# Kernel optimization log

Measured on AMD Instinct MI355X. Metric: run time of the kernel, lower is better.

Reference implementation:

```python
import jax, jax.numpy as jnp
import numpy as np

B, L, DIM = 2, 2048, 1024
H, D = 16, 64  # n_heads, head_dim; H*D == DIM


def setup_inputs() -> dict:
    key = jax.random.key(0)
    ks = jax.random.split(key, 5)
    s = 0.02
    return {
        "x": jax.random.normal(ks[0], (B, L, DIM), dtype=jnp.float32),
        "Wq": jax.random.normal(ks[1], (DIM, H * D), dtype=jnp.float32) * s,
        "Wk": jax.random.normal(ks[2], (DIM, H * D), dtype=jnp.float32) * s,
        "Wv": jax.random.normal(ks[3], (DIM, H * D), dtype=jnp.float32) * s,
        "Wo": jax.random.normal(ks[4], (H * D, DIM), dtype=jnp.float32) * s,
    }


def reference(x, Wq, Wk, Wv, Wo):
    b, l, _ = x.shape
    scale = 1.0 / np.sqrt(D).astype(np.float32)
    # QKV projections -> [b, h, l, d]
    q = (x @ Wq).reshape(b, l, H, D).transpose(0, 2, 1, 3)
    k = (x @ Wk).reshape(b, l, H, D).transpose(0, 2, 1, 3)
    v = (x @ Wv).reshape(b, l, H, D).transpose(0, 2, 1, 3)
    # dense scores [b, h, l, l]
    scores = jnp.einsum("bhqd,bhkd->bhqk", q, k)
    # diagonal mask: each token cannot attend to itself
    diag = jnp.eye(l, dtype=bool)  # [l, l]
    scores = jnp.where(diag, -jnp.inf, scores)
    attn = jax.nn.softmax(scores * scale, axis=-1)
    out = jnp.einsum("bhqk,bhkd->bhqd", attn, v)
    out = out.transpose(0, 2, 1, 3).reshape(b, l, H * D)
    return out @ Wo
```

## Files before the change

kernel.cpp:

```cpp
#include <hip/hip_runtime.h>
#include <hip/hip_bf16.h>
#include <math.h>

#define L_SEQ 2048
#define DIMN  1024
#define NH    16
#define HD    64
#define NB    2
#define NTOK  (NB * L_SEQ)

typedef __attribute__((ext_vector_type(8))) short bf16x8;
typedef __attribute__((ext_vector_type(4))) float f32x4;
typedef __attribute__((ext_vector_type(4))) short short4v;
typedef __attribute__((ext_vector_type(2))) unsigned uint32x2;

__device__ __forceinline__ short f2bf(float x) {
  return (short)__bfloat16_as_ushort(__float2bfloat16(x));
}

__device__ __forceinline__ unsigned cvt_pk_bf16(float lo, float hi) {
  unsigned r;
  asm("v_cvt_pk_bf16_f32 %0, %1, %2" : "=v"(r) : "v"(lo), "v"(hi));
  return r;
}

__device__ __forceinline__ void gload_lds16(const short* gsrc, char* lds_dst) {
  __builtin_amdgcn_global_load_lds(
      (const __attribute__((address_space(1))) void*)gsrc,
      (__attribute__((address_space(3))) void*)lds_dst, 16, 0, 0);
}

__global__ __launch_bounds__(256) void cast_x_k(const float* __restrict__ in,
                                                short* __restrict__ out) {
  const int i = (blockIdx.x * 256 + threadIdx.x) * 8;
  float4 a = *(const float4*)(in + i);
  float4 b = *(const float4*)(in + i + 4);
  bf16x8 o;
  o[0] = f2bf(a.x); o[1] = f2bf(a.y); o[2] = f2bf(a.z); o[3] = f2bf(a.w);
  o[4] = f2bf(b.x); o[5] = f2bf(b.y); o[6] = f2bf(b.z); o[7] = f2bf(b.w);
  *(bf16x8*)(out + i) = o;
}

__global__ __launch_bounds__(256) void castT_k(const float* __restrict__ W,
                                               short* __restrict__ Wt) {
  __shared__ float s[64][65];
  const int tid = threadIdx.x;
  const int k0 = blockIdx.y * 64, n0 = blockIdx.x * 64;
#pragma unroll
  for (int i = 0; i < 4; ++i) {
    int idx = i * 256 + tid;
    int r = idx >> 4, c = (idx & 15) * 4;
    float4 v = *(const float4*)(W + (size_t)(k0 + r) * DIMN + n0 + c);
    s[r][c] = v.x; s[r][c + 1] = v.y; s[r][c + 2] = v.z; s[r][c + 3] = v.w;
  }
  __syncthreads();
#pragma unroll
  for (int i = 0; i < 4; ++i) {
    int idx = i * 256 + tid;
    int r = idx >> 4, c = (idx & 15) * 4;
    short4v o = { f2bf(s[c][r]), f2bf(s[c + 1][r]), f2bf(s[c + 2][r]), f2bf(s[c + 3][r]) };
    *(short4v*)(Wt + (size_t)(n0 + r) * DIMN + k0 + c) = o;
  }
}

__global__ __launch_bounds__(256) void vT_k(const short* __restrict__ V,
                                            short* __restrict__ Vt) {
  __shared__ short s[64][72];
  const int tid = threadIdx.x;
  const int bh = blockIdx.y;
  const int l0 = blockIdx.x * 64;
  const int row = tid >> 2, c0 = (tid & 3) * 16;
  const short* Vh = V + (size_t)bh * L_SEQ * HD;
  bf16x8 a = *(const bf16x8*)(Vh + (size_t)(l0 + row) * HD + c0);
  bf16x8 b = *(const bf16x8*)(Vh + (size_t)(l0 + row) * HD + c0 + 8);
#pragma unroll
  for (int j = 0; j < 8; ++j) { s[c0 + j][row] = a[j]; s[c0 + 8 + j][row] = b[j]; }
  __syncthreads();
  short* Vth = Vt + (size_t)bh * HD * L_SEQ;
  bf16x8 o0 = *(const bf16x8*)&s[row][c0];
  bf16x8 o1 = *(const bf16x8*)&s[row][c0 + 8];
  *(bf16x8*)(Vth + (size_t)row * L_SEQ + l0 + c0) = o0;
  *(bf16x8*)(Vth + (size_t)row * L_SEQ + l0 + c0 + 8) = o1;
}

template <int MODE>
__global__ __launch_bounds__(256) void mm_k(const short* __restrict__ A,
                                            const short* __restrict__ B0,
                                            const short* __restrict__ B1,
                                            const short* __restrict__ B2,
                                            void* __restrict__ C0,
                                            void* __restrict__ C1,
                                            void* __restrict__ C2,
                                            float scale0) {
  __shared__ char smem[65536];
  const int tid  = threadIdx.x;
  const int lane = tid & 63, wv = tid >> 6;
  const int g = lane >> 4, r16 = lane & 15;
  const int wr = wv >> 1, wc = wv & 1;
  const int row0 = blockIdx.y * 128, col0 = blockIdx.x * 128;
  const int z = blockIdx.z;
  const short* Bt = (z == 0) ? B0 : (z == 1 ? B1 : B2);
  const float scale = (MODE == 0 && z == 0) ? scale0 : 1.0f;

  f32x4 acc[4][4];
#pragma unroll
  for (int mi = 0; mi < 4; ++mi)
#pragma unroll
    for (int ni = 0; ni < 4; ++ni) acc[mi][ni] = (f32x4){0.f, 0.f, 0.f, 0.f};

  auto stage = [&](int buf, int kt) {
    const int k0 = kt * 64;
    char* As = smem + buf * 32768;
    char* Bs = As + 16384;
#pragma unroll
    for (int j = 0; j < 4; ++j) {
      const int o = j * 4096 + wv * 1024 + lane * 16;
      const int row = o >> 7;
      const int slot = (o >> 4) & 7;
      const int ksrc = k0 + ((slot ^ (row & 7)) << 3);
      gload_lds16(A  + (size_t)(row0 + row) * DIMN + ksrc, As + j * 4096 + wv * 1024);
      gload_lds16(Bt + (size_t)(col0 + row) * DIMN + ksrc, Bs + j * 4096 + wv * 1024);
    }
  };

  auto compute = [&](int buf) {
    const char* As = smem + buf * 32768;
    const char* Bs = As + 16384;
#pragma unroll
    for (int ks = 0; ks < 2; ++ks) {
      bf16x8 a[4], b[4];
#pragma unroll
      for (int mi = 0; mi < 4; ++mi) {
        const int row = wr * 64 + mi * 16 + r16;
        const int slot = (ks * 4 + g) ^ (row & 7);
        a[mi] = *(const bf16x8*)(As + row * 128 + slot * 16);
      }
#pragma unroll
      for (int ni = 0; ni < 4; ++ni) {
        const int row = wc * 64 + ni * 16 + r16;
        const int slot = (ks * 4 + g) ^ (row & 7);
        b[ni] = *(const bf16x8*)(Bs + row * 128 + slot * 16);
      }
#pragma unroll
      for (int mi = 0; mi < 4; ++mi)
#pragma unroll
        for (int ni = 0; ni < 4; ++ni)
          acc[mi][ni] = __builtin_amdgcn_mfma_f32_16x16x32_bf16(a[mi], b[ni], acc[mi][ni], 0, 0, 0);
    }
  };

  stage(0, 0);
  __syncthreads();
  int cur = 0;
  for (int kt = 0; kt < DIMN / 64 - 1; ++kt) {
    stage(cur ^ 1, kt + 1);
    compute(cur);
    __syncthreads();
    cur ^= 1;
  }
  compute(cur);

  void* Cp = (z == 0) ? C0 : (z == 1 ? C1 : C2);
#pragma unroll
  for (int mi = 0; mi < 4; ++mi) {
#pragma unroll
    for (int reg = 0; reg < 4; ++reg) {
      const int t = row0 + wr * 64 + mi * 16 + 4 * g + reg;
#pragma unroll
      for (int ni = 0; ni < 4; ++ni) {
        const int n = col0 + wc * 64 + ni * 16 + r16;
        if (MODE == 0) {
          const int b = t >> 11, l = t & (L_SEQ - 1);
          const int h = n >> 6, d = n & 63;
          ((short*)Cp)[(((size_t)(b * NH + h)) * L_SEQ + l) * HD + d] =
              f2bf(acc[mi][ni][reg] * scale);
        } else {
          ((float*)Cp)[(size_t)t * DIMN + n] = acc[mi][ni][reg];
        }
      }
    }
  }
}

__global__ __launch_bounds__(256) void attn_k(const short* __restrict__ Q,
                                              const short* __restrict__ K,
                                              const short* __restrict__ Vt,
                                              short* __restrict__ O) {
  __shared__ char kv[2][16384];
  __shared__ __align__(16) short Ps[4][16][64];

  const int tid  = threadIdx.x;
  const int wave = tid >> 6, lane = tid & 63;
  const int g = lane >> 4, r16 = lane & 15;
  const int bh = blockIdx.y, qtile = blockIdx.x;
  const int qbase = qtile * 64 + wave * 16;

  const short* Qh  = Q  + (size_t)bh * L_SEQ * HD;
  const short* Kh  = K  + (size_t)bh * L_SEQ * HD;
  const short* Vth = Vt + (size_t)bh * HD * L_SEQ;

  bf16x8 bq[2];
  bq[0] = *(const bf16x8*)(Qh + (size_t)(qbase + r16) * HD + 8 * g);
  bq[1] = *(const bf16x8*)(Qh + (size_t)(qbase + r16) * HD + 8 * g + 32);

  float lsum = 0.f;
  f32x4 o[4];
#pragma unroll
  for (int db = 0; db < 4; ++db) o[db] = (f32x4){0.f, 0.f, 0.f, 0.f};

  const int sw = r16 & 15 & 7;
  char* PsRow = (char*)Ps + wave * 2048 + r16 * 128;
  char* pw_addr[4];
#pragma unroll
  for (int kb = 0; kb < 4; ++kb) {
    const int gi = (2 * kb + (g >> 1)) ^ sw;
    pw_addr[kb] = PsRow + gi * 16 + (g & 1) * 8;
  }
  const char* bp_addr[2] = { PsRow + ((0 + g) ^ sw) * 16,
                             PsRow + ((4 + g) ^ sw) * 16 };
  const int slk0 = ((0 + g) ^ sw) * 16;
  const int slk1 = ((4 + g) ^ sw) * 16;
  const int rbase = r16 * 128;

  const int si1 = 256 + tid;
  const int row0s = tid >> 3,  c0s = (((tid & 7) ^ (row0s & 7)) << 3);
  const int row1s = si1 >> 3,  c1s = (((si1 & 7) ^ (row1s & 7)) << 3);
  const short* kp0 = Kh + (size_t)row0s * HD + c0s;
  const short* kp1 = Kh + (size_t)row1s * HD + c1s;
  const short* vp0 = Vth + (size_t)row0s * L_SEQ + c0s;
  const short* vp1 = Vth + (size_t)row1s * L_SEQ + c1s;
  const int ldo0 = tid * 16, ldo1 = si1 * 16;

  auto stage = [&](int buf) {
    char* base = kv[buf];
    gload_lds16(kp0, base + ldo0);
    gload_lds16(kp1, base + ldo1);
    gload_lds16(vp0, base + 8192 + ldo0);
    gload_lds16(vp1, base + 8192 + ldo1);
    kp0 += 64 * HD;
    kp1 += 64 * HD;
    vp0 += 64;
    vp1 += 64;
  };

  auto compute = [&](int buf, int kt) {
    const char* Kb = kv[buf];
    const char* Vb = kv[buf] + 8192;

    f32x4 s[4];
#pragma unroll
    for (int kb = 0; kb < 4; ++kb) s[kb] = (f32x4){0.f, 0.f, 0.f, 0.f};
    __builtin_amdgcn_s_setprio(1);
#pragma unroll
    for (int kb = 0; kb < 4; ++kb) {
      bf16x8 ak0 = *(const bf16x8*)(Kb + rbase + kb * 2048 + slk0);
      s[kb] = __builtin_amdgcn_mfma_f32_16x16x32_bf16(ak0, bq[0], s[kb], 0, 0, 0);
      bf16x8 ak1 = *(const bf16x8*)(Kb + rbase + kb * 2048 + slk1);
      s[kb] = __builtin_amdgcn_mfma_f32_16x16x32_bf16(ak1, bq[1], s[kb], 0, 0, 0);
    }
    __builtin_amdgcn_s_setprio(0);

    if (kt == qtile) {
      const int qg = qbase + r16;
#pragma unroll
      for (int kb = 0; kb < 4; ++kb)
#pragma unroll
        for (int r = 0; r < 4; ++r)
          if (kt * 64 + kb * 16 + 4 * g + r == qg) s[kb][r] = -INFINITY;
    }

#pragma unroll
    for (int kb = 0; kb < 4; ++kb)
#pragma unroll
      for (int r = 0; r < 4; ++r) s[kb][r] = exp2f(s[kb][r]);
    float t0 = (s[0][0] + s[0][1]) + (s[0][2] + s[0][3]);
    float t1 = (s[1][0] + s[1][1]) + (s[1][2] + s[1][3]);
    float t2 = (s[2][0] + s[2][1]) + (s[2][2] + s[2][3]);
    float t3 = (s[3][0] + s[3][1]) + (s[3][2] + s[3][3]);
    lsum += (t0 + t1) + (t2 + t3);

#pragma unroll
    for (int kb = 0; kb < 4; ++kb) {
      uint32x2 pw = { cvt_pk_bf16(s[kb][0], s[kb][1]),
                      cvt_pk_bf16(s[kb][2], s[kb][3]) };
      *(uint32x2*)pw_addr[kb] = pw;
    }

    __builtin_amdgcn_s_setprio(1);
#pragma unroll
    for (int ks = 0; ks < 2; ++ks) {
      bf16x8 bp = *(const bf16x8*)bp_addr[ks];
      const int sl = ks ? slk1 : slk0;
#pragma unroll
      for (int db = 0; db < 4; ++db) {
        bf16x8 av = *(const bf16x8*)(Vb + rbase + db * 2048 + sl);
        o[db] = __builtin_amdgcn_mfma_f32_16x16x32_bf16(av, bp, o[db], 0, 0, 0);
      }
    }
    __builtin_amdgcn_s_setprio(0);
  };

  stage(0);
  __syncthreads();

  for (int t = 0; t < L_SEQ / 64; t += 2) {
    stage(1);
    compute(0, t);
    __syncthreads();
    if (t + 2 < L_SEQ / 64) stage(0);
    compute(1, t + 1);
    __syncthreads();
  }

  lsum += __shfl_xor(lsum, 16);
  lsum += __shfl_xor(lsum, 32);

  const int b = bh >> 4, h = bh & 15;
  const float inv = 1.0f / lsum;
  const size_t rowO = (size_t)(b * L_SEQ + qbase + r16) * DIMN + h * HD;
#pragma unroll
  for (int db = 0; db < 4; ++db) {
    uint32x2 ow = { cvt_pk_bf16(o[db][0] * inv, o[db][1] * inv),
                    cvt_pk_bf16(o[db][2] * inv, o[db][3] * inv) };
    *(uint32x2*)(O + rowO + db * 16 + 4 * g) = ow;
  }
}

extern "C" void kernel_launch(void* const* d_in, const int* in_sizes, int n_in,
                              void* d_out, int out_size, void* d_ws, size_t ws_size,
                              hipStream_t stream) {
  const float* x  = (const float*)d_in[0];
  const float* Wq = (const float*)d_in[1];
  const float* Wk = (const float*)d_in[2];
  const float* Wv = (const float*)d_in[3];
  const float* Wo = (const float*)d_in[4];
  float* out = (float*)d_out;

  short* xb  = (short*)d_ws;
  short* Wqt = xb  + (size_t)NTOK * DIMN;
  short* Wkt = Wqt + (size_t)DIMN * DIMN;
  short* Wvt = Wkt + (size_t)DIMN * DIMN;
  short* Wot = Wvt + (size_t)DIMN * DIMN;
  short* Qb  = Wot + (size_t)DIMN * DIMN;
  short* Kb  = Qb  + (size_t)NTOK * DIMN;
  short* Vb  = Kb  + (size_t)NTOK * DIMN;
  short* Vtb = Vb  + (size_t)NTOK * DIMN;
  short* AO  = Vtb + (size_t)NTOK * DIMN;

  cast_x_k<<<NTOK * DIMN / (256 * 8), 256, 0, stream>>>(x, xb);
  const dim3 tgrid(DIMN / 64, DIMN / 64);
  castT_k<<<tgrid, 256, 0, stream>>>(Wq, Wqt);
  castT_k<<<tgrid, 256, 0, stream>>>(Wk, Wkt);
  castT_k<<<tgrid, 256, 0, stream>>>(Wv, Wvt);
  castT_k<<<tgrid, 256, 0, stream>>>(Wo, Wot);

  mm_k<0><<<dim3(DIMN / 128, NTOK / 128, 3), 256, 0, stream>>>(
      xb, Wqt, Wkt, Wvt, Qb, Kb, Vb, 0.125f * 1.4426950408889634f);

  vT_k<<<dim3(L_SEQ / 64, NB * NH), 256, 0, stream>>>(Vb, Vtb);

  attn_k<<<dim3(L_SEQ / 64, NB * NH), 256, 0, stream>>>(Qb, Kb, Vtb, AO);

  mm_k<1><<<dim3(DIMN / 128, NTOK / 128, 1), 256, 0, stream>>>(
      AO, Wot, Wot, Wot, out, out, out, 1.0f);
}
```

Measured before the change: 140.5 us.

## Use 32x32 MFMA in attention with register-only P via permlane32 swap

```diff
diff --git a/kernel.cpp b/kernel.cpp
--- a/kernel.cpp
+++ b/kernel.cpp
@@ -11,6 +11,7 @@
 
 typedef __attribute__((ext_vector_type(8))) short bf16x8;
 typedef __attribute__((ext_vector_type(4))) float f32x4;
+typedef __attribute__((ext_vector_type(16))) float f32x16;
 typedef __attribute__((ext_vector_type(4))) short short4v;
 typedef __attribute__((ext_vector_type(2))) unsigned uint32x2;
 
@@ -22,6 +23,10 @@
   unsigned r;
   asm("v_cvt_pk_bf16_f32 %0, %1, %2" : "=v"(r) : "v"(lo), "v"(hi));
   return r;
+}
+
+__device__ __forceinline__ void permlane32_swap(unsigned& a, unsigned& b) {
+  asm volatile("v_permlane32_swap_b32 %0, %1" : "+v"(a), "+v"(b));
 }
 
 __device__ __forceinline__ void gload_lds16(const short* gsrc, char* lds_dst) {
@@ -187,40 +192,33 @@
                                               const short* __restrict__ Vt,
                                               short* __restrict__ O) {
   __shared__ char kv[2][16384];
-  __shared__ __align__(16) short Ps[4][16][64];
 
   const int tid  = threadIdx.x;
   const int wave = tid >> 6, lane = tid & 63;
-  const int g = lane >> 4, r16 = lane & 15;
+  const int h = lane >> 5, r32 = lane & 31;
   const int bh = blockIdx.y, qtile = blockIdx.x;
-  const int qbase = qtile * 64 + wave * 16;
+  const int qbase = qtile * 128 + wave * 32;
+  const int dtile = qtile * 2 + (wave >> 1);
+  const int qg = qbase + r32;
 
   const short* Qh  = Q  + (size_t)bh * L_SEQ * HD;
   const short* Kh  = K  + (size_t)bh * L_SEQ * HD;
   const short* Vth = Vt + (size_t)bh * HD * L_SEQ;
 
-  bf16x8 bq[2];
-  bq[0] = *(const bf16x8*)(Qh + (size_t)(qbase + r16) * HD + 8 * g);
-  bq[1] = *(const bf16x8*)(Qh + (size_t)(qbase + r16) * HD + 8 * g + 32);
+  bf16x8 qv[4];
+#pragma unroll
+  for (int ks = 0; ks < 4; ++ks)
+    qv[ks] = *(const bf16x8*)(Qh + (size_t)qg * HD + ks * 16 + 8 * h);
 
   float lsum = 0.f;
-  f32x4 o[4];
-#pragma unroll
-  for (int db = 0; db < 4; ++db) o[db] = (f32x4){0.f, 0.f, 0.f, 0.f};
-
-  const int sw = r16 & 15 & 7;
-  char* PsRow = (char*)Ps + wave * 2048 + r16 * 128;
-  char* pw_addr[4];
-#pragma unroll
-  for (int kb = 0; kb < 4; ++kb) {
-    const int gi = (2 * kb + (g >> 1)) ^ sw;
-    pw_addr[kb] = PsRow + gi * 16 + (g & 1) * 8;
-  }
-  const char* bp_addr[2] = { PsRow + ((0 + g) ^ sw) * 16,
-                             PsRow + ((4 + g) ^ sw) * 16 };
-  const int slk0 = ((0 + g) ^ sw) * 16;
-  const int slk1 = ((4 + g) ^ sw) * 16;
-  const int rbase = r16 * 128;
+  f32x16 o32[2];
+#pragma unroll
+  for (int db = 0; db < 2; ++db)
+#pragma unroll
+    for (int r = 0; r < 16; ++r) o32[db][r] = 0.f;
+
+  const int sw = r32 & 7;
+  const int rbase = r32 * 128;
 
   const int si1 = 256 + tid;
   const int row0s = tid >> 3,  c0s = (((tid & 7) ^ (row0s & 7)) << 3);
@@ -247,56 +245,68 @@
     const char* Kb = kv[buf];
     const char* Vb = kv[buf] + 8192;
 
-    f32x4 s[4];
-#pragma unroll
-    for (int kb = 0; kb < 4; ++kb) s[kb] = (f32x4){0.f, 0.f, 0.f, 0.f};
+    f32x16 sa[2];
+#pragma unroll
+    for (int kb = 0; kb < 2; ++kb)
+#pragma unroll
+      for (int r = 0; r < 16; ++r) sa[kb][r] = 0.f;
     __builtin_amdgcn_s_setprio(1);
 #pragma unroll
-    for (int kb = 0; kb < 4; ++kb) {
-      bf16x8 ak0 = *(const bf16x8*)(Kb + rbase + kb * 2048 + slk0);
-      s[kb] = __builtin_amdgcn_mfma_f32_16x16x32_bf16(ak0, bq[0], s[kb], 0, 0, 0);
-      bf16x8 ak1 = *(const bf16x8*)(Kb + rbase + kb * 2048 + slk1);
-      s[kb] = __builtin_amdgcn_mfma_f32_16x16x32_bf16(ak1, bq[1], s[kb], 0, 0, 0);
-    }
+    for (int kb = 0; kb < 2; ++kb)
+#pragma unroll
+      for (int ks = 0; ks < 4; ++ks) {
+        bf16x8 ak = *(const bf16x8*)(Kb + (kb * 32) * 128 + rbase + ((2 * ks + h) ^ sw) * 16);
+        sa[kb] = __builtin_amdgcn_mfma_f32_32x32x16_bf16(ak, qv[ks], sa[kb], 0, 0, 0);
+      }
     __builtin_amdgcn_s_setprio(0);
 
-    if (kt == qtile) {
-      const int qg = qbase + r16;
-#pragma unroll
-      for (int kb = 0; kb < 4; ++kb)
-#pragma unroll
-        for (int r = 0; r < 4; ++r)
-          if (kt * 64 + kb * 16 + 4 * g + r == qg) s[kb][r] = -INFINITY;
-    }
-
-#pragma unroll
-    for (int kb = 0; kb < 4; ++kb)
-#pragma unroll
-      for (int r = 0; r < 4; ++r) s[kb][r] = exp2f(s[kb][r]);
-    float t0 = (s[0][0] + s[0][1]) + (s[0][2] + s[0][3]);
-    float t1 = (s[1][0] + s[1][1]) + (s[1][2] + s[1][3]);
-    float t2 = (s[2][0] + s[2][1]) + (s[2][2] + s[2][3]);
-    float t3 = (s[3][0] + s[3][1]) + (s[3][2] + s[3][3]);
-    lsum += (t0 + t1) + (t2 + t3);
-
-#pragma unroll
-    for (int kb = 0; kb < 4; ++kb) {
-      uint32x2 pw = { cvt_pk_bf16(s[kb][0], s[kb][1]),
-                      cvt_pk_bf16(s[kb][2], s[kb][3]) };
-      *(uint32x2*)pw_addr[kb] = pw;
+    if (kt == dtile) {
+      const int tgt = qg - kt * 64;
+#pragma unroll
+      for (int kb = 0; kb < 2; ++kb)
+#pragma unroll
+        for (int r = 0; r < 16; ++r)
+          if (kb * 32 + (r & 3) + 8 * (r >> 2) + 4 * h == tgt) sa[kb][r] = -INFINITY;
+    }
+
+#pragma unroll
+    for (int kb = 0; kb < 2; ++kb)
+#pragma unroll
+      for (int r = 0; r < 16; ++r) sa[kb][r] = exp2f(sa[kb][r]);
+    float ps = 0.f;
+#pragma unroll
+    for (int kb = 0; kb < 2; ++kb) {
+      float u0 = (sa[kb][0] + sa[kb][1]) + (sa[kb][2] + sa[kb][3]);
+      float u1 = (sa[kb][4] + sa[kb][5]) + (sa[kb][6] + sa[kb][7]);
+      float u2 = (sa[kb][8] + sa[kb][9]) + (sa[kb][10] + sa[kb][11]);
+      float u3 = (sa[kb][12] + sa[kb][13]) + (sa[kb][14] + sa[kb][15]);
+      ps += (u0 + u1) + (u2 + u3);
+    }
+    lsum += ps;
+
+    bf16x8 bp[4];
+#pragma unroll
+    for (int kk = 0; kk < 4; ++kk) {
+      const int kb = kk >> 1, s8 = (kk & 1) * 8;
+      unsigned lo0 = cvt_pk_bf16(sa[kb][s8 + 0], sa[kb][s8 + 1]);
+      unsigned lo1 = cvt_pk_bf16(sa[kb][s8 + 2], sa[kb][s8 + 3]);
+      unsigned hi0 = cvt_pk_bf16(sa[kb][s8 + 4], sa[kb][s8 + 5]);
+      unsigned hi1 = cvt_pk_bf16(sa[kb][s8 + 6], sa[kb][s8 + 7]);
+      permlane32_swap(lo0, hi0);
+      permlane32_swap(lo1, hi1);
+      union { unsigned w[4]; bf16x8 v; } u;
+      u.w[0] = lo0; u.w[1] = lo1; u.w[2] = hi0; u.w[3] = hi1;
+      bp[kk] = u.v;
     }
 
     __builtin_amdgcn_s_setprio(1);
 #pragma unroll
-    for (int ks = 0; ks < 2; ++ks) {
-      bf16x8 bp = *(const bf16x8*)bp_addr[ks];
-      const int sl = ks ? slk1 : slk0;
-#pragma unroll
-      for (int db = 0; db < 4; ++db) {
-        bf16x8 av = *(const bf16x8*)(Vb + rbase + db * 2048 + sl);
-        o[db] = __builtin_amdgcn_mfma_f32_16x16x32_bf16(av, bp, o[db], 0, 0, 0);
-      }
-    }
+    for (int kk = 0; kk < 4; ++kk)
+#pragma unroll
+      for (int db = 0; db < 2; ++db) {
+        bf16x8 av = *(const bf16x8*)(Vb + (db * 32) * 128 + rbase + ((2 * kk + h) ^ sw) * 16);
+        o32[db] = __builtin_amdgcn_mfma_f32_32x32x16_bf16(av, bp[kk], o32[db], 0, 0, 0);
+      }
     __builtin_amdgcn_s_setprio(0);
   };
 
@@ -312,18 +322,20 @@
     __syncthreads();
   }
 
-  lsum += __shfl_xor(lsum, 16);
   lsum += __shfl_xor(lsum, 32);
 
-  const int b = bh >> 4, h = bh & 15;
+  const int b = bh >> 4, hh = bh & 15;
   const float inv = 1.0f / lsum;
-  const size_t rowO = (size_t)(b * L_SEQ + qbase + r16) * DIMN + h * HD;
-#pragma unroll
-  for (int db = 0; db < 4; ++db) {
-    uint32x2 ow = { cvt_pk_bf16(o[db][0] * inv, o[db][1] * inv),
-                    cvt_pk_bf16(o[db][2] * inv, o[db][3] * inv) };
-    *(uint32x2*)(O + rowO + db * 16 + 4 * g) = ow;
-  }
+  const size_t rowO = (size_t)(b * L_SEQ + qg) * DIMN + hh * HD;
+#pragma unroll
+  for (int db = 0; db < 2; ++db)
+#pragma unroll
+    for (int grp = 0; grp < 4; ++grp) {
+      const int d0 = db * 32 + grp * 8 + 4 * h;
+      uint32x2 ow = { cvt_pk_bf16(o32[db][grp * 4 + 0] * inv, o32[db][grp * 4 + 1] * inv),
+                      cvt_pk_bf16(o32[db][grp * 4 + 2] * inv, o32[db][grp * 4 + 3] * inv) };
+      *(uint32x2*)(O + rowO + d0) = ow;
+    }
 }
 
 extern "C" void kernel_launch(void* const* d_in, const int* in_sizes, int n_in,
@@ -359,7 +371,7 @@
 
   vT_k<<<dim3(L_SEQ / 64, NB * NH), 256, 0, stream>>>(Vb, Vtb);
 
-  attn_k<<<dim3(L_SEQ / 64, NB * NH), 256, 0, stream>>>(Qb, Kb, Vtb, AO);
+  attn_k<<<dim3(L_SEQ / 128, NB * NH), 256, 0, stream>>>(Qb, Kb, Vtb, AO);
 
   mm_k<1><<<dim3(DIMN / 128, NTOK / 128, 1), 256, 0, stream>>>(
       AO, Wot, Wot, Wot, out, out, out, 1.0f);
```

After: 140.2 us. No clear change (-0.2%).
